# Performance work log

Hardware: AMD Instinct MI355X
Metric: run time of the kernel (lower is better)

Reference implementation:

```python
import jax, jax.numpy as jnp
import numpy as np

B, S, D, H = 64, 1024, 256, 256


def setup_inputs() -> dict:
    key = jax.random.key(0)
    k1, k2, k3, k4, k5 = jax.random.split(key, 5)
    stdv = 1.0 / np.sqrt(H)
    x = jax.random.normal(k1, (B, S, D), dtype=jnp.float32)
    modality_lambda = jax.random.uniform(k2, (S,), dtype=jnp.float32)
    W = jax.random.uniform(k3, (D, 4 * H), minval=-stdv, maxval=stdv, dtype=jnp.float32)
    U = jax.random.uniform(k4, (H, 4 * H), minval=-stdv, maxval=stdv, dtype=jnp.float32)
    bias = jax.random.uniform(k5, (4 * H,), minval=-stdv, maxval=stdv, dtype=jnp.float32)
    return {"x": x, "modality_lambda": modality_lambda, "W": W, "U": U, "bias": bias}


def reference(x, modality_lambda, W, U, bias):
    hs = U.shape[0]
    bs = x.shape[0]
    # Precompute input projection for all timesteps in one GEMM: [S, B, 4H]
    x_proj = jnp.einsum('bsd,dg->sbg', x, W) + bias
    h0 = jnp.zeros((bs, hs), x.dtype)
    c0 = jnp.zeros((bs, hs), x.dtype)

    def step(carry, inp):
        h, c = carry
        xp, lam = inp
        gates = xp + h @ U  # [B, 4H]
        i_t = jax.nn.sigmoid(gates[:, :hs])
        f_t = jax.nn.sigmoid(gates[:, hs:2 * hs])
        g_t = jnp.tanh(gates[:, 2 * hs:3 * hs])
        o_t = jax.nn.sigmoid(gates[:, 3 * hs:])
        c = f_t * c + i_t * g_t * lam
        h = o_t * jnp.tanh(c)
        return (h, c), h

    (h_t, c_t), hidden_seq = jax.lax.scan(step, (h0, c0), (x_proj, modality_lambda))
    hidden_seq = jnp.transpose(hidden_seq, (1, 0, 2))  # [B, S, H]
    return hidden_seq, h_t, c_t
```

## Files before the change

### kernel.cpp

```cpp
#include <hip/hip_runtime.h>
#include <hip/hip_bf16.h>


#define BSH 16777216u
#define BH  16384u

typedef short short8 __attribute__((ext_vector_type(8)));
typedef float float4_ __attribute__((ext_vector_type(4)));
typedef unsigned int uint2_ __attribute__((ext_vector_type(2)));
typedef unsigned int uint4_ __attribute__((ext_vector_type(4)));

static __device__ __forceinline__ unsigned short f2bf(float f) {
    unsigned int u = __builtin_bit_cast(unsigned int, f);
    u += 0x7FFFu + ((u >> 16) & 1u);
    return (unsigned short)(u >> 16);
}
static __device__ __forceinline__ float bf2f(unsigned short h) {
    unsigned int u = ((unsigned int)h) << 16;
    return __builtin_bit_cast(float, u);
}
static __device__ __forceinline__ uint4_ pack8(const unsigned short* t) {
    uint4_ v;
    v.x = (unsigned int)t[0] | ((unsigned int)t[1] << 16);
    v.y = (unsigned int)t[2] | ((unsigned int)t[3] << 16);
    v.z = (unsigned int)t[4] | ((unsigned int)t[5] << 16);
    v.w = (unsigned int)t[6] | ((unsigned int)t[7] << 16);
    return v;
}
static __device__ __forceinline__ unsigned umin_(unsigned a, unsigned b) {
    return a < b ? a : b;
}
static __device__ __forceinline__ void gload_lds16(const void* g, void* l) {
    __builtin_amdgcn_global_load_lds(
        (const __attribute__((address_space(1))) unsigned int*)g,
        (__attribute__((address_space(3))) unsigned int*)l, 16, 0, 0);
}
static __device__ __forceinline__ void barrier_lgkm() {
    asm volatile("s_waitcnt lgkmcnt(0)" ::: "memory");
    __builtin_amdgcn_s_barrier();
    asm volatile("" ::: "memory");
}

__global__ void prep_kernel(const float* __restrict__ W, const float* __restrict__ U,
                            const float* __restrict__ bias,
                            unsigned short* __restrict__ Wbf, unsigned short* __restrict__ Ubf,
                            float* __restrict__ biasf) {
    int tid = blockIdx.x * blockDim.x + threadIdx.x;
    if (tid < 65536) {
        int idx = tid & 32767;
        const bool isU = (tid >= 32768);
        const float* src = isU ? U : W;
        unsigned short* dst = isU ? Ubf : Wbf;
        int sl = idx >> 9, kt = (idx >> 6) & 7, lane = idx & 63;
        int c = lane & 15, kgrp = lane >> 4;
        int m = sl >> 3, wv = sl & 7;
        int gatec = c >> 2, jj = c & 3;
        int ncol = gatec * 256 + 32 * m + 4 * wv + jj;
        unsigned short t8[8];
#pragma unroll
        for (int e = 0; e < 8; e++) {
            int k = kt * 32 + kgrp * 8 + e;
            float v = src[k * 1024 + ncol];
            t8[e] = f2bf(isU ? -v : v);
        }
        *(uint4_*)(dst + (size_t)idx * 8) = pack8(t8);
    } else if (tid < 66560) {
        int idx2 = tid - 65536;
        int sl = idx2 >> 4, c = idx2 & 15;
        int m = sl >> 3, wv = sl & 7, gatec = c >> 2, jj = c & 3;
        int ncol = gatec * 256 + 32 * m + 4 * wv + jj;
        biasf[idx2] = bias[ncol];
    }
}

__global__ __launch_bounds__(512, 2)
void xproj_kernel(const float* __restrict__ x, const unsigned short* __restrict__ Wbf,
                  const float* __restrict__ biasf, unsigned short* __restrict__ xp) {
    const int bx = blockIdx.x;
    const int g = bx & 3, tile = bx >> 2;
    const int s0 = tile * 4;
    const int tidx = threadIdx.x;
    const int w = tidx >> 6, lane = tidx & 63;

    __shared__ unsigned short Afrag[4][8][64][8];

    {
        int row = tidx >> 3;
        int kt = tidx & 7;
        int si = row >> 4, r = row & 15;
        int b = g * 16 + r, s = s0 + si;
        const float* px = x + ((size_t)b * 1024 + s) * 256 + kt * 32;
#pragma unroll
        for (int kg = 0; kg < 4; kg++) {
            float4_ v0 = *(const float4_*)(px + kg * 8);
            float4_ v1 = *(const float4_*)(px + kg * 8 + 4);
            unsigned short t8[8] = { f2bf(v0.x), f2bf(v0.y), f2bf(v0.z), f2bf(v0.w),
                                     f2bf(v1.x), f2bf(v1.y), f2bf(v1.z), f2bf(v1.w) };
            *(uint4_*)&Afrag[si][kt][kg * 16 + r][0] = pack8(t8);
        }
    }
    __syncthreads();

    float4_ acc[8][4];
#pragma unroll
    for (int q = 0; q < 8; q++) {
        int sl = w * 8 + q;
        float bv = biasf[sl * 16 + (lane & 15)];
#pragma unroll
        for (int si = 0; si < 4; si++) acc[q][si] = (float4_){bv, bv, bv, bv};
    }
#pragma unroll
    for (int kt = 0; kt < 8; kt++) {
        short8 a[4];
#pragma unroll
        for (int si = 0; si < 4; si++)
            a[si] = *(const short8*)&Afrag[si][kt][lane][0];
#pragma unroll
        for (int q = 0; q < 8; q++) {
            short8 bfr = *(const short8*)(Wbf + (((size_t)(w * 8 + q) * 8 + kt) * 64 + lane) * 8);
#pragma unroll
            for (int si = 0; si < 4; si++)
                acc[q][si] = __builtin_amdgcn_mfma_f32_16x16x32_bf16(a[si], bfr, acc[q][si], 0, 0, 0);
        }
    }
#pragma unroll
    for (int q = 0; q < 8; q++) {
        int sl = w * 8 + q;
        int wgx = g * 8 + (sl >> 3);
#pragma unroll
        for (int si = 0; si < 4; si++) {
            int s = s0 + si;
            unsigned int lo = (unsigned int)f2bf(acc[q][si].x) | ((unsigned int)f2bf(acc[q][si].y) << 16);
            unsigned int hi = (unsigned int)f2bf(acc[q][si].z) | ((unsigned int)f2bf(acc[q][si].w) << 16);
            uint2_ v = {lo, hi};
            *(uint2_*)(xp + ((((size_t)wgx * 1024 + s) * 8 + (sl & 7)) * 64 + lane) * 4) = v;
        }
    }
}

__global__ __launch_bounds__(576, 1)
void lstm_kernel(const unsigned short* __restrict__ Ubf,
                 const unsigned short* __restrict__ xp,
                 const float* __restrict__ lam,
                 unsigned short* __restrict__ hbuf,
                 float* __restrict__ out) {
    const int bx = blockIdx.x;
    const int g = bx & 3;
    const int m = bx >> 2;
    const int tid = threadIdx.x;
    const int w = tid >> 6, lane = tid & 63;

    __shared__ float lamLDS[1024];
    __shared__ alignas(16) unsigned short htmp[2][16][40];
    __shared__ alignas(16) unsigned short xpring[8][2048];
    __shared__ alignas(16) unsigned short hstage[2][8][64][8];

    for (int i = tid; i < 1024; i += 576) lamLDS[i] = lam[i];

    const int col = lane & 15;
    const int gatec = col >> 2, jj = col & 3;
    const int rr0 = (lane >> 4) * 4;
    const bool active = (gatec == 0);

    short8 u[8];
    if (w < 8) {
        int sl = m * 8 + w;
#pragma unroll
        for (int kt = 0; kt < 8; kt++)
            u[kt] = *(const short8*)(Ubf + (((size_t)sl * 8 + kt) * 64 + lane) * 8);
    }

    const size_t wgx = (size_t)(g * 8 + m);

    if (w == 8) {
        for (int s = 0; s < 6; s++) {
            const char* src = (const char*)xp + ((wgx * 1024 + s) << 12) + (size_t)lane * 16;
            char* dst = (char*)&xpring[s][0];
#pragma unroll
            for (int c2 = 0; c2 < 4; c2++)
                gload_lds16(src + c2 * 1024, dst + c2 * 1024);
        }
        asm volatile("s_waitcnt vmcnt(20)" ::: "memory");
    }

    float cst[4] = {0.f, 0.f, 0.f, 0.f};
    barrier_lgkm();

    char* hpub = (char*)hbuf + ((size_t)g << 13) + (size_t)m * 1024
               + (size_t)((w >> 1) * 256 + (w & 1) * 8) + (size_t)lane * 16;
    const char* pb = (const char*)hbuf + ((size_t)g << 13) + (size_t)w * 1024
                   + (size_t)lane * 16 - 32768;

    for (int t = 0; t < 1024; t++) {
        if (w < 8) {
            if (t > 0) {
                uint4_ r;
                for (;;) {
                    asm volatile("global_load_dwordx4 %0, %1, off sc0 sc1\n\t"
                                 "s_waitcnt vmcnt(0)"
                                 : "=v"(r) : "v"(pb) : "memory");
                    __builtin_amdgcn_sched_barrier(0);
                    if (__all(umin_(umin_(r.x, r.y), umin_(r.z, r.w)) != 0u)) break;
                }
                *(uint4_*)&hstage[t & 1][w][lane][0] = r;
            }
        } else if (w == 8) {
            if (t + 6 < 1024) {
                int slot = (t + 6) & 7;
                const char* src = (const char*)xp + ((wgx * 1024 + (size_t)(t + 6)) << 12)
                                  + (size_t)lane * 16;
                char* dst = (char*)&xpring[slot][0];
#pragma unroll
                for (int c2 = 0; c2 < 4; c2++)
                    gload_lds16(src + c2 * 1024, dst + c2 * 1024);
            }
            if (t == 0)            asm volatile("s_waitcnt vmcnt(20)" ::: "memory");
            else if (t == 1)       asm volatile("s_waitcnt vmcnt(22)" ::: "memory");
            else if (t + 6 < 1024) asm volatile("s_waitcnt vmcnt(24)" ::: "memory");
            else                   asm volatile("s_waitcnt vmcnt(0)"  ::: "memory");
        }
        barrier_lgkm();
        if (w < 8) {
            unsigned long long xpd =
                *(const unsigned long long*)&xpring[t & 7][w * 256 + lane * 4];
            float4_ acc0, acc1 = (float4_){0.f, 0.f, 0.f, 0.f};
            acc0.x = bf2f((unsigned short)(xpd & 0xffff));
            acc0.y = bf2f((unsigned short)((xpd >> 16) & 0xffff));
            acc0.z = bf2f((unsigned short)((xpd >> 32) & 0xffff));
            acc0.w = bf2f((unsigned short)(xpd >> 48));

            if (t > 0) {
                short8 a0 = *(const short8*)&hstage[t & 1][0][lane][0];
                short8 a1 = *(const short8*)&hstage[t & 1][1][lane][0];
                short8 a2 = *(const short8*)&hstage[t & 1][2][lane][0];
                short8 a3 = *(const short8*)&hstage[t & 1][3][lane][0];
                short8 a4 = *(const short8*)&hstage[t & 1][4][lane][0];
                short8 a5 = *(const short8*)&hstage[t & 1][5][lane][0];
                short8 a6 = *(const short8*)&hstage[t & 1][6][lane][0];
                short8 a7 = *(const short8*)&hstage[t & 1][7][lane][0];
                acc0 = __builtin_amdgcn_mfma_f32_16x16x32_bf16(a0, u[0], acc0, 0, 0, 0);
                acc1 = __builtin_amdgcn_mfma_f32_16x16x32_bf16(a1, u[1], acc1, 0, 0, 0);
                acc0 = __builtin_amdgcn_mfma_f32_16x16x32_bf16(a2, u[2], acc0, 0, 0, 0);
                acc1 = __builtin_amdgcn_mfma_f32_16x16x32_bf16(a3, u[3], acc1, 0, 0, 0);
                acc0 = __builtin_amdgcn_mfma_f32_16x16x32_bf16(a4, u[4], acc0, 0, 0, 0);
                acc1 = __builtin_amdgcn_mfma_f32_16x16x32_bf16(a5, u[5], acc1, 0, 0, 0);
                acc0 = __builtin_amdgcn_mfma_f32_16x16x32_bf16(a6, u[6], acc0, 0, 0, 0);
                acc1 = __builtin_amdgcn_mfma_f32_16x16x32_bf16(a7, u[7], acc1, 0, 0, 0);
            }

            float lamt = lamLDS[t];
            float gv[4], fv[4], ggv[4], ov[4];
#pragma unroll
            for (int q = 0; q < 4; q++) {
                float xg = acc0[q] + acc1[q];
                float y = (gatec == 2) ? 2.f * xg : xg;
                float sgm = 1.f / (1.f + __expf(-y));
                gv[q] = (gatec == 2) ? 2.f * sgm - 1.f : sgm;
            }
#pragma unroll
            for (int q = 0; q < 4; q++) {
                fv[q]  = __shfl(gv[q], lane + 4, 64);
                ggv[q] = __shfl(gv[q], lane + 8, 64);
                ov[q]  = __shfl(gv[q], lane + 12, 64);
            }
            if (active) {
                float hq[4];
#pragma unroll
                for (int q = 0; q < 4; q++) {
                    float c = fv[q] * cst[q] + gv[q] * ggv[q] * lamt;
                    cst[q] = c;
                    float th = 2.f / (1.f + __expf(-2.f * c)) - 1.f;
                    hq[q] = ov[q] * th;
                    unsigned short b = f2bf(-hq[q]);
                    if (b == 0) b = 0x8000u;
                    htmp[t & 1][rr0 + q][4 * w + jj] = b;
                }
                if (t == 1023) {
#pragma unroll
                    for (int q = 0; q < 4; q++) {
                        size_t b = (size_t)g * 16 + rr0 + q;
                        int j = m * 32 + 4 * w + jj;
                        out[BSH + b * 256 + j] = hq[q];
                        out[BSH + BH + b * 256 + j] = cst[q];
                    }
                }
            }
            asm volatile("s_waitcnt lgkmcnt(0)" ::: "memory");
            if (lane < 16) {
                uint2_ chunk = *(const uint2_*)&htmp[t & 1][lane][4 * w];
                asm volatile("global_store_dwordx2 %0, %1, off sc0 sc1"
                             :: "v"(hpub), "v"(chunk) : "memory");
            }
        } else if (w == 8) {
            if (t > 0) {
                int r = lane >> 2, seg = lane & 3;
                uint4_ hv = *(const uint4_*)&htmp[(t - 1) & 1][r][seg * 8];
                hv.x ^= 0x80008000u; hv.y ^= 0x80008000u;
                hv.z ^= 0x80008000u; hv.w ^= 0x80008000u;
                float4_ v0 = { bf2f((unsigned short)(hv.x & 0xffff)), bf2f((unsigned short)(hv.x >> 16)),
                               bf2f((unsigned short)(hv.y & 0xffff)), bf2f((unsigned short)(hv.y >> 16)) };
                float4_ v1 = { bf2f((unsigned short)(hv.z & 0xffff)), bf2f((unsigned short)(hv.z >> 16)),
                               bf2f((unsigned short)(hv.w & 0xffff)), bf2f((unsigned short)(hv.w >> 16)) };
                float* po = out + (((size_t)(g * 16 + r)) << 18) + ((size_t)(t - 1) << 8)
                            + m * 32 + seg * 8;
                *(float4_*)po = v0;
                *(float4_*)(po + 4) = v1;
            }
        }
        pb += 32768;
        hpub += 32768;
    }
    barrier_lgkm();
    if (w == 8) {
        int r = lane >> 2, seg = lane & 3;
        uint4_ hv = *(const uint4_*)&htmp[1][r][seg * 8];
        hv.x ^= 0x80008000u; hv.y ^= 0x80008000u;
        hv.z ^= 0x80008000u; hv.w ^= 0x80008000u;
        float4_ v0 = { bf2f((unsigned short)(hv.x & 0xffff)), bf2f((unsigned short)(hv.x >> 16)),
                       bf2f((unsigned short)(hv.y & 0xffff)), bf2f((unsigned short)(hv.y >> 16)) };
        float4_ v1 = { bf2f((unsigned short)(hv.z & 0xffff)), bf2f((unsigned short)(hv.z >> 16)),
                       bf2f((unsigned short)(hv.w & 0xffff)), bf2f((unsigned short)(hv.w >> 16)) };
        float* po = out + (((size_t)(g * 16 + r)) << 18) + ((size_t)1023 << 8) + m * 32 + seg * 8;
        *(float4_*)po = v0;
        *(float4_*)(po + 4) = v1;
    }
}

__global__ void ws_too_small_kernel(float* out) {
    if (threadIdx.x == 0 && blockIdx.x == 0) out[0] = -777777.0f;
}

extern "C" void kernel_launch(void* const* d_in, const int* in_sizes, int n_in,
                              void* d_out, int out_size, void* d_ws, size_t ws_size,
                              hipStream_t stream) {
    const float* x    = (const float*)d_in[0];
    const float* lam  = (const float*)d_in[1];
    const float* W    = (const float*)d_in[2];
    const float* U    = (const float*)d_in[3];
    const float* bias = (const float*)d_in[4];
    float* out = (float*)d_out;

    const size_t NEED = (size_t)162 << 20;
    if (ws_size < NEED) {
        ws_too_small_kernel<<<1, 64, 0, stream>>>(out);
        return;
    }
    char* ws = (char*)d_ws;
    unsigned short* Ubf   = (unsigned short*)(ws + (256 << 10));
    unsigned short* Wbf   = (unsigned short*)(ws + (768 << 10));
    float*          biasf = (float*)(ws + (1280 << 10));
    unsigned short* hbuf  = (unsigned short*)(ws + ((size_t)2 << 20));
    unsigned short* xp    = (unsigned short*)(ws + ((size_t)34 << 20));

    hipMemsetAsync(hbuf, 0, (size_t)32 << 20, stream);
    prep_kernel<<<260, 256, 0, stream>>>(W, U, bias, Wbf, Ubf, biasf);
    xproj_kernel<<<1024, 512, 0, stream>>>(x, Wbf, biasf, xp);
    lstm_kernel<<<32, 576, 0, stream>>>(Ubf, xp, lam, hbuf, out);
}
```

Before: 2.224 ms.

## Add fast-path h exchange with per-element publishing and a dedicated publisher wave

Adds a second hidden-state exchange buffer. Active lanes write their bf16 h values straight to global memory with sc0-only stores, and consumers poll that buffer with sc0 loads, avoiding the LDS gather and the fully coherent store before publishing. A new tenth wave polls LDS for the complete h tile, writes the coherent slow copy and the fp32 output, then clears the tile. This takes the output writes and the slow publish off the critical compute waves. Consumers fall back to the slow coherent buffer if the fast poll times out, because sc0-only coherence across CUs is uncertain. The launch grows to 64 blocks with half exiting at once, presumably to spread blocks across XCDs, and each block zero-fills the fast buffer in the prologue.

```diff
diff --git a/kernel.cpp b/kernel.cpp
--- a/kernel.cpp
+++ b/kernel.cpp
@@ -29,6 +29,11 @@
 }
 static __device__ __forceinline__ unsigned umin_(unsigned a, unsigned b) {
     return a < b ? a : b;
+}
+static __device__ __forceinline__ unsigned pkmin16(unsigned a, unsigned b) {
+    unsigned d;
+    asm("v_pk_min_u16 %0, %1, %2" : "=v"(d) : "v"(a), "v"(b));
+    return d;
 }
 static __device__ __forceinline__ void gload_lds16(const void* g, void* l) {
     __builtin_amdgcn_global_load_lds(
@@ -138,15 +143,17 @@
     }
 }
 
-__global__ __launch_bounds__(576, 1)
+__global__ __launch_bounds__(640, 1)
 void lstm_kernel(const unsigned short* __restrict__ Ubf,
                  const unsigned short* __restrict__ xp,
                  const float* __restrict__ lam,
-                 unsigned short* __restrict__ hbuf,
+                 unsigned short* __restrict__ hslow,
+                 unsigned short* __restrict__ hfast,
                  float* __restrict__ out) {
     const int bx = blockIdx.x;
-    const int g = bx & 3;
-    const int m = bx >> 2;
+    const int g = bx & 7;
+    if (g >= 4) return;
+    const int m = bx >> 3;
     const int tid = threadIdx.x;
     const int w = tid >> 6, lane = tid & 63;
 
@@ -155,12 +162,14 @@
     __shared__ alignas(16) unsigned short xpring[8][2048];
     __shared__ alignas(16) unsigned short hstage[2][8][64][8];
 
-    for (int i = tid; i < 1024; i += 576) lamLDS[i] = lam[i];
+    ((unsigned int*)htmp)[tid] = 0u;
+    for (int i = tid; i < 1024; i += 640) lamLDS[i] = lam[i];
 
     const int col = lane & 15;
     const int gatec = col >> 2, jj = col & 3;
     const int rr0 = (lane >> 4) * 4;
     const bool active = (gatec == 0);
+    const bool fast_en = (hfast != nullptr);
 
     short8 u[8];
     if (w < 8) {
@@ -171,6 +180,15 @@
     }
 
     const size_t wgx = (size_t)(g * 8 + m);
+
+    if (w < 8 && fast_en) {
+        char* pz = (char*)hfast + ((size_t)g << 13) + (size_t)w * 1024 + (size_t)lane * 16;
+        uint4_ z = {0u, 0u, 0u, 0u};
+        for (int tt = 0; tt < 1024; tt++) {
+            asm volatile("global_store_dwordx4 %0, %1, off sc0" :: "v"(pz), "v"(z) : "memory");
+            pz += 32768;
+        }
+    }
 
     if (w == 8) {
         for (int s = 0; s < 6; s++) {
@@ -186,21 +204,43 @@
     float cst[4] = {0.f, 0.f, 0.f, 0.f};
     barrier_lgkm();
 
-    char* hpub = (char*)hbuf + ((size_t)g << 13) + (size_t)m * 1024
-               + (size_t)((w >> 1) * 256 + (w & 1) * 8) + (size_t)lane * 16;
-    const char* pb = (const char*)hbuf + ((size_t)g << 13) + (size_t)w * 1024
+    const int u_col = 4 * w + jj;
+    char* hpubF = (char*)hfast + ((size_t)g << 13) + (size_t)m * 1024
+                + (size_t)((u_col >> 3) * 256 + rr0 * 16 + (u_col & 7) * 2);
+    const char* pf = (const char*)hfast + ((size_t)g << 13) + (size_t)w * 1024
                    + (size_t)lane * 16 - 32768;
+    const char* pb = (const char*)hslow + ((size_t)g << 13) + (size_t)w * 1024
+                   + (size_t)lane * 16 - 32768;
+    char* hps = (char*)hslow + ((size_t)g << 13) + (size_t)m * 1024 + (size_t)lane * 16;
+
+    bool use_fast = fast_en;
 
     for (int t = 0; t < 1024; t++) {
         if (w < 8) {
             if (t > 0) {
                 uint4_ r;
-                for (;;) {
-                    asm volatile("global_load_dwordx4 %0, %1, off sc0 sc1\n\t"
-                                 "s_waitcnt vmcnt(0)"
-                                 : "=v"(r) : "v"(pb) : "memory");
-                    __builtin_amdgcn_sched_barrier(0);
-                    if (__all(umin_(umin_(r.x, r.y), umin_(r.z, r.w)) != 0u)) break;
+                bool got = false;
+                if (use_fast) {
+                    for (int k = 0; k < 12; k++) {
+                        asm volatile("global_load_dwordx4 %0, %1, off sc0\n\t"
+                                     "s_waitcnt vmcnt(0)"
+                                     : "=v"(r) : "v"(pf) : "memory");
+                        __builtin_amdgcn_sched_barrier(0);
+                        unsigned mm = pkmin16(pkmin16(r.x, r.y), pkmin16(r.z, r.w));
+                        if (__all(((mm & 0xffffu) != 0u) && ((mm >> 16) != 0u))) {
+                            got = true; break;
+                        }
+                    }
+                    if (!got && t > 8) use_fast = false;
+                }
+                if (!got) {
+                    for (;;) {
+                        asm volatile("global_load_dwordx4 %0, %1, off sc0 sc1\n\t"
+                                     "s_waitcnt vmcnt(0)"
+                                     : "=v"(r) : "v"(pb) : "memory");
+                        __builtin_amdgcn_sched_barrier(0);
+                        if (__all(umin_(umin_(r.x, r.y), umin_(r.z, r.w)) != 0u)) break;
+                    }
                 }
                 *(uint4_*)&hstage[t & 1][w][lane][0] = r;
             }
@@ -265,6 +305,7 @@
             }
             if (active) {
                 float hq[4];
+                unsigned short hb[4];
 #pragma unroll
                 for (int q = 0; q < 4; q++) {
                     float c = fv[q] * cst[q] + gv[q] * ggv[q] * lamt;
@@ -273,8 +314,17 @@
                     hq[q] = ov[q] * th;
                     unsigned short b = f2bf(-hq[q]);
                     if (b == 0) b = 0x8000u;
-                    htmp[t & 1][rr0 + q][4 * w + jj] = b;
+                    hb[q] = b;
                 }
+                if (fast_en) {
+                    asm volatile("global_store_short %0, %1, off sc0"           :: "v"(hpubF), "v"((unsigned)hb[0]) : "memory");
+                    asm volatile("global_store_short %0, %1, off offset:16 sc0" :: "v"(hpubF), "v"((unsigned)hb[1]) : "memory");
+                    asm volatile("global_store_short %0, %1, off offset:32 sc0" :: "v"(hpubF), "v"((unsigned)hb[2]) : "memory");
+                    asm volatile("global_store_short %0, %1, off offset:48 sc0" :: "v"(hpubF), "v"((unsigned)hb[3]) : "memory");
+                }
+#pragma unroll
+                for (int q = 0; q < 4; q++)
+                    htmp[t & 1][rr0 + q][4 * w + jj] = hb[q];
                 if (t == 1023) {
 #pragma unroll
                     for (int q = 0; q < 4; q++) {
@@ -285,44 +335,36 @@
                     }
                 }
             }
-            asm volatile("s_waitcnt lgkmcnt(0)" ::: "memory");
-            if (lane < 16) {
-                uint2_ chunk = *(const uint2_*)&htmp[t & 1][lane][4 * w];
-                asm volatile("global_store_dwordx2 %0, %1, off sc0 sc1"
-                             :: "v"(hpub), "v"(chunk) : "memory");
-            }
-        } else if (w == 8) {
-            if (t > 0) {
-                int r = lane >> 2, seg = lane & 3;
-                uint4_ hv = *(const uint4_*)&htmp[(t - 1) & 1][r][seg * 8];
-                hv.x ^= 0x80008000u; hv.y ^= 0x80008000u;
-                hv.z ^= 0x80008000u; hv.w ^= 0x80008000u;
-                float4_ v0 = { bf2f((unsigned short)(hv.x & 0xffff)), bf2f((unsigned short)(hv.x >> 16)),
-                               bf2f((unsigned short)(hv.y & 0xffff)), bf2f((unsigned short)(hv.y >> 16)) };
-                float4_ v1 = { bf2f((unsigned short)(hv.z & 0xffff)), bf2f((unsigned short)(hv.z >> 16)),
-                               bf2f((unsigned short)(hv.w & 0xffff)), bf2f((unsigned short)(hv.w >> 16)) };
-                float* po = out + (((size_t)(g * 16 + r)) << 18) + ((size_t)(t - 1) << 8)
-                            + m * 32 + seg * 8;
-                *(float4_*)po = v0;
-                *(float4_*)(po + 4) = v1;
-            }
-        }
+        } else if (w == 9) {
+            int r_ = lane & 15, kg = lane >> 4;
+            volatile unsigned int* hp32 =
+                (volatile unsigned int*)&htmp[t & 1][r_][kg * 8];
+            unsigned a0, a1, a2, a3;
+            for (;;) {
+                a0 = hp32[0]; a1 = hp32[1]; a2 = hp32[2]; a3 = hp32[3];
+                unsigned mm = pkmin16(pkmin16(a0, a1), pkmin16(a2, a3));
+                if (__all(((mm & 0xffffu) != 0u) && ((mm >> 16) != 0u))) break;
+            }
+            uint4_ blk = {a0, a1, a2, a3};
+            asm volatile("global_store_dwordx4 %0, %1, off sc0 sc1"
+                         :: "v"(hps), "v"(blk) : "memory");
+            unsigned x0 = a0 ^ 0x80008000u, x1 = a1 ^ 0x80008000u;
+            unsigned x2 = a2 ^ 0x80008000u, x3 = a3 ^ 0x80008000u;
+            float4_ v0 = { bf2f((unsigned short)(x0 & 0xffff)), bf2f((unsigned short)(x0 >> 16)),
+                           bf2f((unsigned short)(x1 & 0xffff)), bf2f((unsigned short)(x1 >> 16)) };
+            float4_ v1 = { bf2f((unsigned short)(x2 & 0xffff)), bf2f((unsigned short)(x2 >> 16)),
+                           bf2f((unsigned short)(x3 & 0xffff)), bf2f((unsigned short)(x3 >> 16)) };
+            float* po = out + (((size_t)(g * 16 + r_)) << 18) + ((size_t)t << 8)
+                        + m * 32 + kg * 8;
+            *(float4_*)po = v0;
+            *(float4_*)(po + 4) = v1;
+            uint4_ z = {0u, 0u, 0u, 0u};
+            *(uint4_*)&htmp[t & 1][r_][kg * 8] = z;
+        }
+        pf += 32768;
         pb += 32768;
-        hpub += 32768;
-    }
-    barrier_lgkm();
-    if (w == 8) {
-        int r = lane >> 2, seg = lane & 3;
-        uint4_ hv = *(const uint4_*)&htmp[1][r][seg * 8];
-        hv.x ^= 0x80008000u; hv.y ^= 0x80008000u;
-        hv.z ^= 0x80008000u; hv.w ^= 0x80008000u;
-        float4_ v0 = { bf2f((unsigned short)(hv.x & 0xffff)), bf2f((unsigned short)(hv.x >> 16)),
-                       bf2f((unsigned short)(hv.y & 0xffff)), bf2f((unsigned short)(hv.y >> 16)) };
-        float4_ v1 = { bf2f((unsigned short)(hv.z & 0xffff)), bf2f((unsigned short)(hv.z >> 16)),
-                       bf2f((unsigned short)(hv.w & 0xffff)), bf2f((unsigned short)(hv.w >> 16)) };
-        float* po = out + (((size_t)(g * 16 + r)) << 18) + ((size_t)1023 << 8) + m * 32 + seg * 8;
-        *(float4_*)po = v0;
-        *(float4_*)(po + 4) = v1;
+        hpubF += 32768;
+        hps += 32768;
     }
 }
 
@@ -340,20 +382,25 @@
     const float* bias = (const float*)d_in[4];
     float* out = (float*)d_out;
 
-    const size_t NEED = (size_t)162 << 20;
-    if (ws_size < NEED) {
+    const size_t NEED_BASE = (size_t)162 << 20;
+    const size_t NEED_FAST = (size_t)194 << 20;
+    if (ws_size < NEED_BASE) {
         ws_too_small_kernel<<<1, 64, 0, stream>>>(out);
         return;
     }
+    const bool fast_en = (ws_size >= NEED_FAST);
     char* ws = (char*)d_ws;
     unsigned short* Ubf   = (unsigned short*)(ws + (256 << 10));
     unsigned short* Wbf   = (unsigned short*)(ws + (768 << 10));
     float*          biasf = (float*)(ws + (1280 << 10));
-    unsigned short* hbuf  = (unsigned short*)(ws + ((size_t)2 << 20));
-    unsigned short* xp    = (unsigned short*)(ws + ((size_t)34 << 20));
-
-    hipMemsetAsync(hbuf, 0, (size_t)32 << 20, stream);
+    unsigned short* hslow = (unsigned short*)(ws + ((size_t)2 << 20));
+    unsigned short* xp    = (unsigned short*)(ws + ((size_t)66 << 20));
+    unsigned short* hfast = fast_en ? (unsigned short*)(ws + ((size_t)34 << 20)) : nullptr;
+
+    hipMemsetAsync(hslow, 0, (size_t)32 << 20, stream);
+    if (fast_en)
+        hipMemsetAsync(hfast, 0, (size_t)32 << 20, stream);
     prep_kernel<<<260, 256, 0, stream>>>(W, U, bias, Wbf, Ubf, biasf);
     xproj_kernel<<<1024, 512, 0, stream>>>(x, Wbf, biasf, xp);
-    lstm_kernel<<<32, 576, 0, stream>>>(Ubf, xp, lam, hbuf, out);
-}
+    lstm_kernel<<<64, 640, 0, stream>>>(Ubf, xp, lam, hslow, hfast, out);
+}
```

New measurement: 2.079 ms. 6.5% less time.
